# Kernel tuning notes

Hardware: AMD Instinct MI355X
Metric: run time of the kernel (lower is better)

The kernel has to match this reference:

```python
import jax, jax.numpy as jnp
import numpy as np
from math import factorial

# ---------------- real Wigner-3j (e3nn-style construction) ----------------

def _su2_cg(j1, j2, j3, m1, m2, m3):
    if m3 != m1 + m2 or not (abs(j1 - j2) <= j3 <= j1 + j2):
        return 0.0
    f = lambda n: float(factorial(n))
    pref = np.sqrt((2 * j3 + 1) * f(j1 + j2 - j3) * f(j1 - j2 + j3) * f(-j1 + j2 + j3) / f(j1 + j2 + j3 + 1))
    pref *= np.sqrt(f(j3 + m3) * f(j3 - m3) * f(j1 - m1) * f(j1 + m1) * f(j2 - m2) * f(j2 + m2))
    vmin = max(0, j2 - j3 - m1, j1 - j3 + m2)
    vmax = min(j1 + j2 - j3, j1 - m1, j2 + m2)
    s = 0.0
    for v in range(vmin, vmax + 1):
        s += (-1) ** v / (f(v) * f(j1 + j2 - j3 - v) * f(j1 - m1 - v) * f(j2 + m2 - v) * f(j3 - j2 + m1 + v) * f(j3 - j1 - m2 + v))
    return pref * s

def _q_real_to_complex(l):
    q = np.zeros((2 * l + 1, 2 * l + 1), dtype=complex)
    for m in range(-l, 0):
        q[l + m, l + abs(m)] = 1 / np.sqrt(2)
        q[l + m, l - abs(m)] = -1j / np.sqrt(2)
    q[l, l] = 1.0
    for m in range(1, l + 1):
        q[l + m, l + abs(m)] = (-1) ** m / np.sqrt(2)
        q[l + m, l - abs(m)] = 1j * (-1) ** m / np.sqrt(2)
    return (-1j) ** l * q

def real_wigner_3j(l1, l2, l3):
    Cc = np.zeros((2 * l1 + 1, 2 * l2 + 1, 2 * l3 + 1), dtype=complex)
    for i, m1 in enumerate(range(-l1, l1 + 1)):
        for j, m2 in enumerate(range(-l2, l2 + 1)):
            for k, m3 in enumerate(range(-l3, l3 + 1)):
                Cc[i, j, k] = _su2_cg(l1, l2, l3, m1, m2, m3)
    Q1, Q2, Q3 = _q_real_to_complex(l1), _q_real_to_complex(l2), _q_real_to_complex(l3)
    C = np.einsum('ia,jb,kc,ijk->abc', Q1, Q2, np.conj(Q3), Cc)
    Cr, Ci = np.real(C), np.imag(C)
    C = Cr if np.abs(Cr).sum() >= np.abs(Ci).sum() else Ci
    n = np.linalg.norm(C)
    return (C / n).astype(np.float32)

# ---------------- module constants ----------------
LMAX = 2
M_TOT = (LMAX + 1) ** 2          # 9
L_SLICES = {0: slice(0, 1), 1: slice(1, 4), 2: slice(4, 9)}
# uvu instruction paths (l1, l2=1, l3) with l3 <= LMAX, parity all even
PATHS = [(0, 1), (1, 0), (1, 1), (1, 2), (2, 1), (2, 2)]
# CG with 'component' irrep normalization: w3j * sqrt(2*l3+1)
W3J = {(l1, l3): real_wigner_3j(l1, 1, l3) * np.sqrt(2 * l3 + 1) for (l1, l3) in PATHS}
COEF1 = 2.04665350914            # E2TensorProduct_FirstOrder.get_coeffs()[1]
SH1_INT = float(np.sqrt(3.0 / (4.0 * np.pi)))  # l=1 'integral' normalization, normalize=False
# element path normalization: counts of paths landing on each output l (1x0e:1, 1e:3, 2e:2)
_counts = np.array([1.0] * 1 + [3.0] * 3 + [2.0] * 5, dtype=np.float32)
PATH_NORM = (1.0 / np.sqrt(_counts)).reshape(1, M_TOT, 1)

# ---------------- building blocks ----------------

def so3_linear(x, W, b):
    # per-degree equivariant linear: x [N, 9, Cin], W [3, Cin, Cout], b [Cout] (l=0 only)
    out = jnp.concatenate([jnp.einsum('nmc,cd->nmd', x[:, L_SLICES[l]], W[l]) for l in range(LMAX + 1)], axis=1)
    return out.at[:, 0, :].add(b)

def tp_uvu(x, y, tp_w):
    # depthwise (uvu) tensor product of x [N, 9, C] with l=1 vector y [N, 3]
    out = jnp.zeros_like(x)
    for p, (l1, l3) in enumerate(PATHS):
        C3 = jnp.asarray(W3J[(l1, l3)])  # [2l1+1, 3, 2l3+1]
        blk = jnp.einsum('abc,nau,nb->ncu', C3, x[:, L_SLICES[l1]], y)
        out = out.at[:, L_SLICES[l3]].add(blk * tp_w[p][None, None, :])
    return out

# ---------------- harness ----------------

def setup_inputs() -> dict:
    key = jax.random.key(0)
    ks = jax.random.split(key, 10)
    N1 = N2 = 4096; K = 16; H = 8; C = 128
    pos = jax.random.normal(ks[0], (N1, 3), dtype=jnp.float32)
    exp_pos = jax.random.normal(ks[1], (N2, 3), dtype=jnp.float32)
    h = jax.random.normal(ks[2], (N1, M_TOT, C), dtype=jnp.float32)
    exp_h = jax.random.normal(ks[3], (N2, M_TOT, C), dtype=jnp.float32)
    alpha_ij = jax.random.uniform(ks[4], (N1, K, H), dtype=jnp.float32)
    f_sparse_idx_expnode = jax.random.randint(ks[5], (N1, K), 0, N2)
    w1_w = jax.random.normal(ks[6], (LMAX + 1, C, C), dtype=jnp.float32) / np.sqrt(C)
    w1_b = jnp.zeros((C,), dtype=jnp.float32)
    w2_w = jax.random.normal(ks[7], (LMAX + 1, C, C), dtype=jnp.float32) / np.sqrt(C)
    w2_b = jnp.zeros((C,), dtype=jnp.float32)
    tp_w = jax.random.normal(ks[8], (len(PATHS), C), dtype=jnp.float32)
    return {"pos": pos, "exp_pos": exp_pos, "h": h, "exp_h": exp_h, "alpha_ij": alpha_ij,
            "f_sparse_idx_expnode": f_sparse_idx_expnode,
            "w1_w": w1_w, "w1_b": w1_b, "w2_w": w2_w, "w2_b": w2_b, "tp_w": tp_w}

def reference(pos, exp_pos, h, exp_h, alpha_ij, f_sparse_idx_expnode, w1_w, w1_b, w2_w, w2_b, tp_w):
    N1, K, H = alpha_ij.shape
    N2, M, C = exp_h.shape
    k = C // H
    exp_h1 = so3_linear(exp_h, w1_w, w1_b)            # w1 (simulated uvw mode)
    y1 = (COEF1 * SH1_INT) * pos                      # Y_powers[1] at target nodes, [N1,3]
    ey1 = (COEF1 * SH1_INT) * exp_pos                 # exp_Y_powers[1], [N2,3]
    # component 1: neighbor-aggregate features, then tensor product with Y(pos)
    gh = exp_h1.reshape(N2, M, H, k)[f_sparse_idx_expnode]          # [N1,K,M,H,k]
    c1 = jnp.einsum('bjh,bjmhk->bmhk', alpha_ij, gh).reshape(N1, M, C)
    c1 = tp_uvu(c1, y1, tp_w)                                       # [N1,M,C]
    # component 2: tensor product at source nodes with Y(exp_pos), then aggregate
    c2 = tp_uvu(exp_h1, ey1, tp_w)                                  # [N2,M,C]
    gc2 = c2.reshape(N2, M, H, k)[f_sparse_idx_expnode]             # [N1,K,M,H,k]
    c2 = jnp.einsum('bjh,bjmhk->bmhk', alpha_ij, gc2).reshape(N1, M, C)
    out = so3_linear(c1 - c2, w2_w, w2_b) * jnp.asarray(PATH_NORM)
    return out
```

## Files before the change

### kernel.cpp

```cpp
#include <hip/hip_runtime.h>

#define NN 4096
#define MTOT 9
#define CH 128

#define S3f 0.57735026918962576f
#define S2f 0.70710678118654752f
#define CUf 0.54772255750516611f
#define CVf 0.31622776601683794f
#define CWf 0.63245553203367587f
#define CAf 0.40824829046386302f
#define CA2f 0.81649658092772603f
#define YSf ((float)(2.04665350914 * 0.48860251190291992))

typedef __attribute__((ext_vector_type(8))) short short8;
typedef __attribute__((ext_vector_type(4))) float f32x4;
typedef __attribute__((ext_vector_type(2))) float f32x2;

__device__ __forceinline__ unsigned short f2b(float f) {
  unsigned u = __builtin_bit_cast(unsigned, f);
  u += 0x7FFFu + ((u >> 16) & 1u);
  return (unsigned short)(u >> 16);
}

__global__ __launch_bounds__(256) void wprep(
    const float* __restrict__ w1, const float* __restrict__ w2,
    unsigned short* __restrict__ o1, unsigned short* __restrict__ o2)
{
  int g = blockIdx.x * 256 + threadIdx.x;
  const float* W = w1;
  unsigned short* O = o1;
  int r = g;
  if (r >= 6144) { r -= 6144; W = w2; O = o2; }
  int l  = r >> 11;
  int r2 = r & 2047;
  int n  = r2 >> 4;
  int kq = r2 & 15;
  const float* src = W + l * 16384 + kq * 8 * CH + n;
  short8 v;
  #pragma unroll
  for (int j = 0; j < 8; ++j) v[j] = (short)f2b(src[j * CH]);
  *(short8*)(O + (size_t)l * 16384 + (((n >> 4) * 16 + kq) * 16 + (n & 15)) * 8) = v;
}

template <int XBF, int YBF, int NORM>
__global__ __launch_bounds__(256) void so3lin_mfma(
    const void* __restrict__ Xv, const unsigned short* __restrict__ Wsw,
    const float* __restrict__ bias, void* __restrict__ Yv)
{
  __shared__ unsigned short Bs[16384];
  const int bid = blockIdx.x;
  int l, blk0, m0, nm;
  if (bid < 64)       { l = 0; blk0 = bid;       m0 = 0; nm = 1; }
  else if (bid < 256) { l = 1; blk0 = bid - 64;  m0 = 1; nm = 3; }
  else                { l = 2; blk0 = bid - 256; m0 = 4; nm = 5; }
  const int t = threadIdx.x;

  {
    const float4* src = (const float4*)(Wsw + (size_t)l * 16384);
    float4* dst = (float4*)Bs;
    #pragma unroll
    for (int i = 0; i < 8; ++i) dst[t + i * 256] = src[t + i * 256];
  }
  __syncthreads();

  const int lane = t & 63;
  const int wave = t >> 6;
  const int c16  = lane & 15;
  const int quad = lane >> 4;
  const int rb   = (blk0 * 4 + wave) * 16;

  const int ra = rb + c16;
  const int nodeA = ra / nm;
  const int mA = m0 + (ra - nodeA * nm);
  const size_t abase = ((size_t)nodeA * MTOT + mA) * CH + quad * 8;

  f32x4 acc[8] = {};
  #pragma unroll
  for (int kk = 0; kk < CH; kk += 32) {
    short8 afrag;
    if (XBF) {
      afrag = *(const short8*)((const unsigned short*)Xv + abase + kk);
    } else {
      const float* xp = (const float*)Xv + abase + kk;
      float4 f0 = *(const float4*)xp;
      float4 f1 = *(const float4*)(xp + 4);
      afrag = (short8){(short)f2b(f0.x), (short)f2b(f0.y), (short)f2b(f0.z), (short)f2b(f0.w),
                       (short)f2b(f1.x), (short)f2b(f1.y), (short)f2b(f1.z), (short)f2b(f1.w)};
    }
    const int kq = (kk >> 3) + quad;
    #pragma unroll
    for (int ct = 0; ct < 8; ++ct) {
      short8 bfrag = *(const short8*)&Bs[((ct * 16 + kq) * 16 + c16) * 8];
      acc[ct] = __builtin_amdgcn_mfma_f32_16x16x32_bf16(afrag, bfrag, acc[ct], 0, 0, 0);
    }
  }

  const float scale = NORM ? (l == 0 ? 1.0f : (l == 1 ? S3f : S2f)) : 1.0f;
  #pragma unroll
  for (int i = 0; i < 4; ++i) {
    int r2 = rb + quad * 4 + i;
    int node2 = r2 / nm;
    int m2 = m0 + (r2 - node2 * nm);
    size_t obase = ((size_t)node2 * MTOT + m2) * CH + c16;
    #pragma unroll
    for (int ct = 0; ct < 8; ++ct) {
      float v = acc[ct][i];
      if (l == 0) v += bias[ct * 16 + c16];
      v *= scale;
      if (YBF) ((unsigned short*)Yv)[obase + ct * 16] = f2b(v);
      else     ((float*)Yv)[obase + ct * 16] = v;
    }
  }
}

__global__ __launch_bounds__(256) void agg_tp_b(
    const unsigned short* __restrict__ X,
    const float* __restrict__ pos,
    const float* __restrict__ exp_pos,
    const float* __restrict__ alpha,
    const int*   __restrict__ idx,
    const float* __restrict__ tpw,
    unsigned short* __restrict__ D)
{
  __shared__ int   sIdx[4][16];
  __shared__ float sAl[4][128];
  __shared__ float sEy[4][48];
  __shared__ float sY[4][4];
  const int t = threadIdx.x, wave = t >> 6, lane = t & 63;
  const int b = blockIdx.x * 4 + wave;

  if (lane < 16) sIdx[wave][lane] = idx[b * 16 + lane];
  sAl[wave][lane]      = alpha[b * 128 + lane];
  sAl[wave][lane + 64] = alpha[b * 128 + lane + 64];
  if (lane < 3) sY[wave][lane] = YSf * pos[b * 3 + lane];
  __syncthreads();
  if (lane < 48) {
    int j = lane / 3, cmp = lane - 3 * j;
    sEy[wave][lane] = YSf * exp_pos[sIdx[wave][j] * 3 + cmp];
  }
  __syncthreads();

  const int h = lane >> 3;
  const int c0 = lane * 2;
  f32x2 A0[9] = {}, A1[9] = {}, A2[9] = {}, A3[9] = {};
  #pragma unroll 2
  for (int j = 0; j < 16; ++j) {
    float al = sAl[wave][j * 8 + h];
    float e0 = al * sEy[wave][j * 3 + 0];
    float e1 = al * sEy[wave][j * 3 + 1];
    float e2 = al * sEy[wave][j * 3 + 2];
    f32x2 alv = {al, al};
    f32x2 e0v = {e0, e0};
    f32x2 e1v = {e1, e1};
    f32x2 e2v = {e2, e2};
    const unsigned short* xp = X + (size_t)sIdx[wave][j] * (MTOT * CH) + c0;
    #pragma unroll
    for (int m = 0; m < 9; ++m) {
      unsigned v = *(const unsigned*)(xp + m * CH);
      f32x2 x;
      x.x = __builtin_bit_cast(float, v << 16);
      x.y = __builtin_bit_cast(float, v & 0xFFFF0000u);
      A0[m] += alv * x; A1[m] += e0v * x; A2[m] += e1v * x; A3[m] += e2v * x;
    }
  }

  const float y0 = sY[wave][0], yv1 = sY[wave][1], y2 = sY[wave][2];
  float OUT[9][2];
  #pragma unroll
  for (int ch = 0; ch < 2; ++ch) {
    const int c = c0 + ch;
    const float w0 = tpw[c], w1 = tpw[CH + c], w2 = tpw[2 * CH + c];
    const float w3 = tpw[3 * CH + c], w4 = tpw[4 * CH + c], w5 = tpw[5 * CH + c];
    const float x0 = A0[0][ch];
    const float p0 = A0[1][ch], p1 = A0[2][ch], p2 = A0[3][ch];
    const float d0 = A0[4][ch], d1 = A0[5][ch], d2 = A0[6][ch], d3 = A0[7][ch], d4 = A0[8][ch];

    float r0 = w1 * S3f * (p0 * y0 + p1 * yv1 + p2 * y2);
    float r1 = w0 * x0 * y0 + w2 * S2f * (p1 * y2 - p2 * yv1)
             + w4 * (CUf * (d0 * y2 + d1 * yv1 - d4 * y0) - CVf * d2 * y0);
    float r2 = w0 * x0 * yv1 + w2 * S2f * (p2 * y0 - p0 * y2)
             + w4 * (CUf * (d1 * y0 + d3 * y2) + CWf * d2 * yv1);
    float r3 = w0 * x0 * y2 + w2 * S2f * (p0 * yv1 - p1 * y0)
             + w4 * (CUf * (d0 * y0 + d4 * y2 + d3 * yv1) - CVf * d2 * y2);
    float r4 = w3 * S2f * (p0 * y2 + p2 * y0)
             + w5 * (CAf * (d3 * y2 - d1 * y0) - 2.f * CAf * d4 * yv1);
    float r5 = w3 * S2f * (p0 * yv1 + p1 * y0)
             + w5 * (CAf * (d0 * y0 - d3 * yv1 + d4 * y2) + S2f * d2 * y2);
    float r6 = w3 * (CA2f * p1 * yv1 - CAf * (p0 * y0 + p2 * y2))
             + w5 * S2f * (d3 * y0 - d1 * y2);
    float r7 = w3 * S2f * (p1 * y2 + p2 * yv1)
             + w5 * (CAf * (d1 * yv1 - d0 * y2 + d4 * y0) - S2f * d2 * y0);
    float r8 = w3 * S2f * (p2 * y2 - p0 * y0)
             + w5 * CAf * (2.f * d0 * yv1 - d1 * y2 - d3 * y0);

    float q0 = w1 * S3f * (A1[1][ch] + A2[2][ch] + A3[3][ch]);
    float q1 = w0 * A1[0][ch] + w2 * S2f * (A3[2][ch] - A2[3][ch])
             + w4 * (CUf * (A3[4][ch] + A2[5][ch] - A1[8][ch]) - CVf * A1[6][ch]);
    float q2 = w0 * A2[0][ch] + w2 * S2f * (A1[3][ch] - A3[1][ch])
             + w4 * (CUf * (A1[5][ch] + A3[7][ch]) + CWf * A2[6][ch]);
    float q3 = w0 * A3[0][ch] + w2 * S2f * (A2[1][ch] - A1[2][ch])
             + w4 * (CUf * (A1[4][ch] + A3[8][ch] + A2[7][ch]) - CVf * A3[6][ch]);
    float q4 = w3 * S2f * (A3[1][ch] + A1[3][ch])
             + w5 * (CAf * (A3[7][ch] - A1[5][ch]) - 2.f * CAf * A2[8][ch]);
    float q5 = w3 * S2f * (A2[1][ch] + A1[2][ch])
             + w5 * (CAf * (A1[4][ch] - A2[7][ch] + A3[8][ch]) + S2f * A3[6][ch]);
    float q6 = w3 * (CA2f * A2[2][ch] - CAf * (A1[1][ch] + A3[3][ch]))
             + w5 * S2f * (A1[7][ch] - A3[5][ch]);
    float q7 = w3 * S2f * (A3[2][ch] + A2[3][ch])
             + w5 * (CAf * (A2[5][ch] - A3[4][ch] + A1[8][ch]) - S2f * A1[6][ch]);
    float q8 = w3 * S2f * (A3[3][ch] - A1[1][ch])
             + w5 * CAf * (2.f * A2[4][ch] - A3[5][ch] - A1[7][ch]);

    OUT[0][ch] = r0 - q0; OUT[1][ch] = r1 - q1; OUT[2][ch] = r2 - q2;
    OUT[3][ch] = r3 - q3; OUT[4][ch] = r4 - q4; OUT[5][ch] = r5 - q5;
    OUT[6][ch] = r6 - q6; OUT[7][ch] = r7 - q7; OUT[8][ch] = r8 - q8;
  }

  #pragma unroll
  for (int m = 0; m < 9; ++m) {
    unsigned dw = (unsigned)f2b(OUT[m][0]) | ((unsigned)f2b(OUT[m][1]) << 16);
    *(unsigned*)(D + ((size_t)b * MTOT + m) * CH + c0) = dw;
  }
}

extern "C" void kernel_launch(void* const* d_in, const int* in_sizes, int n_in,
                              void* d_out, int out_size, void* d_ws, size_t ws_size,
                              hipStream_t stream) {
  (void)in_sizes; (void)n_in; (void)out_size; (void)ws_size;
  const float* pos     = (const float*)d_in[0];
  const float* exp_pos = (const float*)d_in[1];
  const float* exp_h   = (const float*)d_in[3];
  const float* alpha   = (const float*)d_in[4];
  const int*   idx     = (const int*)d_in[5];
  const float* w1w     = (const float*)d_in[6];
  const float* w1b     = (const float*)d_in[7];
  const float* w2w     = (const float*)d_in[8];
  const float* w2b     = (const float*)d_in[9];
  const float* tpw     = (const float*)d_in[10];
  float* out = (float*)d_out;

  unsigned short* eh1 = (unsigned short*)d_ws;
  unsigned short* dif = eh1 + (size_t)NN * MTOT * CH;
  unsigned short* w1s = dif + (size_t)NN * MTOT * CH;
  unsigned short* w2s = w1s + 3 * 16384;

  wprep<<<48, 256, 0, stream>>>(w1w, w2w, w1s, w2s);
  so3lin_mfma<0, 1, 0><<<576, 256, 0, stream>>>(exp_h, w1s, w1b, eh1);
  agg_tp_b<<<NN / 4, 256, 0, stream>>>(eh1, pos, exp_pos, alpha, idx, tpw, dif);
  so3lin_mfma<1, 0, 1><<<576, 256, 0, stream>>>(dif, w2s, w2b, out);
}
```

Baseline: 134.3 us.

## Fuse second SO(3) linear into aggregation/tensor-product kernel via LDS staging

The aggregation + tensor-product kernel now stages its bf16 per-node outputs for 4 nodes into padded shared memory, grouped by l-block. Each wave then runs the w2 MFMA matmul for one l-block and writes the scaled fp32 output directly. This removes the bf16 intermediate buffer round-trip and one kernel launch. In exchange the MFMA tiles are only partly filled, since wave 0 has 4 useful rows and wave 1 has 12. W2 weights are also reloaded by every block, and the extra shared memory may lower occupancy.

After: 139.4 us. 3.8% more time.

```diff
diff --git a/kernel.cpp b/kernel.cpp
--- a/kernel.cpp
+++ b/kernel.cpp
@@ -114,19 +114,23 @@
   }
 }
 
-__global__ __launch_bounds__(256) void agg_tp_b(
+#define PADK 136
+__global__ __launch_bounds__(256) void agg_tp_w2(
     const unsigned short* __restrict__ X,
     const float* __restrict__ pos,
     const float* __restrict__ exp_pos,
     const float* __restrict__ alpha,
     const int*   __restrict__ idx,
     const float* __restrict__ tpw,
-    unsigned short* __restrict__ D)
+    const unsigned short* __restrict__ Wsw,
+    const float* __restrict__ bias,
+    float* __restrict__ out)
 {
   __shared__ int   sIdx[4][16];
   __shared__ float sAl[4][128];
   __shared__ float sEy[4][48];
   __shared__ float sY[4][4];
+  __shared__ __align__(16) unsigned short At[4 * 16 * PADK];
   const int t = threadIdx.x, wave = t >> 6, lane = t & 63;
   const int b = blockIdx.x * 4 + wave;
 
@@ -219,8 +223,50 @@
 
   #pragma unroll
   for (int m = 0; m < 9; ++m) {
+    int tt, rr;
+    if (m == 0)      { tt = 0; rr = wave; }
+    else if (m < 4)  { tt = 1; rr = wave * 3 + (m - 1); }
+    else             { int g = wave * 5 + (m - 4); tt = 2 + (g >> 4); rr = g & 15; }
     unsigned dw = (unsigned)f2b(OUT[m][0]) | ((unsigned)f2b(OUT[m][1]) << 16);
-    *(unsigned*)(D + ((size_t)b * MTOT + m) * CH + c0) = dw;
+    *(unsigned*)&At[(tt * 16 + rr) * PADK + c0] = dw;
+  }
+  __syncthreads();
+
+  const int c16  = lane & 15;
+  const int quad = lane >> 4;
+  const int l2i  = (wave == 0) ? 0 : (wave == 1 ? 1 : 2);
+  const unsigned short* Wl = Wsw + (size_t)l2i * 16384;
+
+  f32x4 acc[8] = {};
+  #pragma unroll
+  for (int kk = 0; kk < CH; kk += 32) {
+    short8 afrag = *(const short8*)&At[(wave * 16 + c16) * PADK + quad * 8 + kk];
+    const int kq = (kk >> 3) + quad;
+    #pragma unroll
+    for (int ct = 0; ct < 8; ++ct) {
+      short8 bfrag = *(const short8*)&Wl[((ct * 16 + kq) * 16 + c16) * 8];
+      acc[ct] = __builtin_amdgcn_mfma_f32_16x16x32_bf16(afrag, bfrag, acc[ct], 0, 0, 0);
+    }
+  }
+
+  const float scale = (wave == 0) ? 1.0f : (wave == 1 ? S3f : S2f);
+  const int rmax = (wave == 1) ? 12 : ((wave == 2) ? 16 : 4);
+  #pragma unroll
+  for (int i = 0; i < 4; ++i) {
+    int rr = quad * 4 + i;
+    if (rr < rmax) {
+      int node, m;
+      if (wave == 0)      { node = rr; m = 0; }
+      else if (wave == 1) { node = rr / 3; m = 1 + rr % 3; }
+      else                { int g = (wave - 2) * 16 + rr; node = g / 5; m = 4 + g % 5; }
+      size_t obase = ((size_t)(blockIdx.x * 4 + node) * MTOT + m) * CH + c16;
+      #pragma unroll
+      for (int ct = 0; ct < 8; ++ct) {
+        float v = acc[ct][i];
+        if (wave == 0) v += bias[ct * 16 + c16];
+        out[obase + ct * 16] = v * scale;
+      }
+    }
   }
 }
 
@@ -241,12 +287,10 @@
   float* out = (float*)d_out;
 
   unsigned short* eh1 = (unsigned short*)d_ws;
-  unsigned short* dif = eh1 + (size_t)NN * MTOT * CH;
-  unsigned short* w1s = dif + (size_t)NN * MTOT * CH;
+  unsigned short* w1s = eh1 + (size_t)NN * MTOT * CH;
   unsigned short* w2s = w1s + 3 * 16384;
 
   wprep<<<48, 256, 0, stream>>>(w1w, w2w, w1s, w2s);
   so3lin_mfma<0, 1, 0><<<576, 256, 0, stream>>>(exp_h, w1s, w1b, eh1);
-  agg_tp_b<<<NN / 4, 256, 0, stream>>>(eh1, pos, exp_pos, alpha, idx, tpw, dif);
-  so3lin_mfma<1, 0, 1><<<576, 256, 0, stream>>>(dif, w2s, w2b, out);
-}
+  agg_tp_w2<<<NN / 4, 256, 0, stream>>>(eh1, pos, exp_pos, alpha, idx, tpw, w2s, w2b, out);
+}
```
